# Optimization experiments

Hardware: AMD Instinct MI355X
Metric: run time of the kernel (lower is better)

The kernel has to match this reference:

```python
import jax, jax.numpy as jnp
import numpy as np

N = 50000       # num nodes
E = 800000      # num edges (avg degree 16)
D_IN = 128
D_H = 128
D_LAT = 64
BN_EPS = 1e-5


def _glorot(key, fan_in, fan_out):
    return jax.random.normal(key, (fan_in, fan_out), jnp.float32) / np.sqrt(fan_in).astype(np.float32)


def setup_inputs() -> dict:
    key = jax.random.key(0)
    ks = jax.random.split(key, 8)
    x = jax.random.normal(ks[0], (N, D_IN), jnp.float32)
    edge_index = jax.random.randint(ks[1], (2, E), 0, N)  # row 0 = src, row 1 = dst
    return {
        "x": x,
        "edge_index": edge_index,
        "W0": _glorot(ks[2], D_IN, D_H),
        "W1": _glorot(ks[3], D_H, D_H),
        "W_mu": _glorot(ks[4], D_H, D_LAT),
        "W_logvar": _glorot(ks[5], D_H, D_LAT),
        "gamma0": jnp.ones((D_H,), jnp.float32),
        "beta0": jnp.zeros((D_H,), jnp.float32),
        "gamma1": jnp.ones((D_H,), jnp.float32),
        "beta1": jnp.zeros((D_H,), jnp.float32),
    }


def _gcn_conv(h, W, src, dst, dinv):
    # Standard GCN with self-loops: D^{-1/2}(A+I)D^{-1/2} (X W)
    m = h @ W                                   # [N, out]
    coef = (dinv[src] * dinv[dst])[:, None]     # [E, 1]
    out = jax.ops.segment_sum(m[src] * coef, dst, num_segments=N)
    return out + m * (dinv * dinv)[:, None]     # self-loop contribution


def _batchnorm(h, gamma, beta):
    mean = jnp.mean(h, axis=0)
    var = jnp.var(h, axis=0)
    return (h - mean) * jax.lax.rsqrt(var + BN_EPS) * gamma + beta


def reference(x, edge_index, W0, W1, W_mu, W_logvar, gamma0, beta0, gamma1, beta1):
    # decoder_type='graph', augment_type=None, used_edge_weight=False,
    # use_FCencoder=False, num_domains=1; dropout is identity in reference.
    src, dst = edge_index[0], edge_index[1]
    deg = jax.ops.segment_sum(jnp.ones((E,), x.dtype), dst, num_segments=N) + 1.0
    dinv = jax.lax.rsqrt(deg)

    h = _gcn_conv(x, W0, src, dst, dinv)
    h = jax.nn.relu(_batchnorm(h, gamma0, beta0))
    h = _gcn_conv(h, W1, src, dst, dinv)
    h = jax.nn.relu(_batchnorm(h, gamma1, beta1))

    z_mean = _gcn_conv(h, W_mu, src, dst, dinv)
    z_log_std = _gcn_conv(h, W_logvar, src, dst, dinv)
    return (z_mean, z_log_std)
```

## Files before the change

### kernel.cpp

```cpp
#include <hip/hip_runtime.h>
#include <hip/hip_bf16.h>


using short8 = __attribute__((ext_vector_type(8))) short;
using f32x4  = __attribute__((ext_vector_type(4))) float;

static __device__ __forceinline__ unsigned short f2bf(float f) {
    __hip_bfloat16 h = __float2bfloat16(f);
    return *reinterpret_cast<unsigned short*>(&h);
}
static __device__ __forceinline__ float bf_lo(unsigned int u) {
    return __uint_as_float(u << 16);
}
static __device__ __forceinline__ float bf_hi(unsigned int u) {
    return __uint_as_float(u & 0xffff0000u);
}
static __device__ __forceinline__ float bf2f(unsigned short u) {
    return __uint_as_float((unsigned int)u << 16);
}

__global__ __launch_bounds__(256)
void deg_count(const int* __restrict__ ei, int* __restrict__ cnt, int E_) {
    int e = blockIdx.x * 256 + threadIdx.x;
    if (e < E_) atomicAdd(&cnt[ei[E_ + e]], 1);
}

__global__ __launch_bounds__(1024)
void scan_blocks(const int* __restrict__ cnt, float* __restrict__ dinv,
                 int* __restrict__ rowptr, int* __restrict__ partials, int n) {
    __shared__ int ls[1024];
    int tid = threadIdx.x;
    int i = blockIdx.x * 1024 + tid;
    int v = (i < n) ? cnt[i] : 0;
    if (i < n) dinv[i] = rsqrtf((float)v + 1.0f);
    ls[tid] = v;
    __syncthreads();
    #pragma unroll
    for (int off = 1; off < 1024; off <<= 1) {
        int t = (tid >= off) ? ls[tid - off] : 0;
        __syncthreads();
        ls[tid] += t;
        __syncthreads();
    }
    if (i < n) rowptr[i] = ls[tid] - v;
    if (tid == 1023) partials[blockIdx.x] = ls[1023];
}

__global__ __launch_bounds__(1024)
void scan_partials(int* __restrict__ partials, int* __restrict__ rowptr_n,
                   int nb) {
    __shared__ int ls[1024];
    int tid = threadIdx.x;
    int v = (tid < nb) ? partials[tid] : 0;
    ls[tid] = v;
    __syncthreads();
    #pragma unroll
    for (int off = 1; off < 1024; off <<= 1) {
        int t = (tid >= off) ? ls[tid - off] : 0;
        __syncthreads();
        ls[tid] += t;
        __syncthreads();
    }
    if (tid < nb) partials[tid] = ls[tid] - v;
    if (tid == 1023) *rowptr_n = ls[1023];
}

__global__ __launch_bounds__(256)
void scan_add(int* __restrict__ rowptr, int* __restrict__ gcursor,
              const int* __restrict__ partials, int n) {
    int i = blockIdx.x * 256 + threadIdx.x;
    if (i < n) {
        int v = rowptr[i] + partials[i >> 10];
        rowptr[i] = v;
        if ((i & 127) == 0) gcursor[i >> 7] = v;
    }
}

#define BCHUNK 4096
__global__ __launch_bounds__(256)
void bin_edges(const int* __restrict__ ei, const float* __restrict__ dinv,
               int* __restrict__ gcursor, uint2* __restrict__ binned, int E_) {
    __shared__ int hist[512];
    __shared__ int gbase[512];
    __shared__ int cur[512];
    const int tid = threadIdx.x;
    const int e0 = blockIdx.x * BCHUNK;

    #pragma unroll
    for (int q = 0; q < 2; ++q) hist[q * 256 + tid] = 0;
    __syncthreads();

    for (int i = tid; i < BCHUNK; i += 256) {
        int e = e0 + i;
        if (e < E_) atomicAdd(&hist[ei[E_ + e] >> 7], 1);
    }
    __syncthreads();

    #pragma unroll
    for (int q = 0; q < 2; ++q) {
        int b = q * 256 + tid;
        int c = hist[b];
        gbase[b] = c ? atomicAdd(&gcursor[b], c) : 0;
        cur[b] = 0;
    }
    __syncthreads();

    for (int i = tid; i < BCHUNK; i += 256) {
        int e = e0 + i;
        if (e >= E_) continue;
        int s = ei[e], d = ei[E_ + e];
        float coef = dinv[s] * dinv[d];
        unsigned int cb = (__float_as_uint(coef) + 0x8000u) >> 16;
        unsigned int entry = ((unsigned int)s << 15) | (cb & 0x7fffu);
        int b = d >> 7;
        int p = gbase[b] + atomicAdd(&cur[b], 1);
        binned[p] = make_uint2(entry, (unsigned int)(d & 127));
    }
}

__global__ __launch_bounds__(256)
void place_edges(const uint2* __restrict__ binned, const int* __restrict__ rowptr,
                 unsigned int* __restrict__ csr, int n) {
    __shared__ int cur[128];
    const int tid = threadIdx.x;
    const int n0 = blockIdx.x * 128;
    const int nn = min(128, n - n0);
    if (tid < nn) cur[tid] = rowptr[n0 + tid];
    __syncthreads();
    const int beg = rowptr[n0];
    const int end = rowptr[min(n0 + 128, n)];
    for (int i = beg + tid; i < end; i += 256) {
        uint2 v = binned[i];
        int p = atomicAdd(&cur[v.y], 1);
        csr[p] = v.x;
    }
}

template<bool XBF, bool FUSE_BN, bool SPLIT_W>
__global__ __launch_bounds__(256)
void gemm_mfma(const void* __restrict__ Xv, const float* __restrict__ Wa,
               const float* __restrict__ Wb, const float* __restrict__ sc,
               const float* __restrict__ sh, unsigned short* __restrict__ Y,
               int nRows) {
    __shared__ unsigned short wt[128 * 128];

    const int tid = threadIdx.x;

    #pragma unroll
    for (int it = 0; it < 16; ++it) {
        int flat4 = it * 256 + tid;
        int k  = flat4 >> 5;
        int c0 = (flat4 & 31) * 4;
        const float* srcp;
        if (!SPLIT_W) srcp = Wa + k * 128 + c0;
        else          srcp = (c0 < 64) ? (Wa + k * 64 + c0)
                                       : (Wb + k * 64 + (c0 - 64));
        float4 v = *(const float4*)srcp;
        float vv[4] = {v.x, v.y, v.z, v.w};
        #pragma unroll
        for (int j = 0; j < 4; ++j) {
            int c = c0 + j;
            wt[c * 128 + (k ^ ((c & 7) << 3))] = f2bf(vv[j]);
        }
    }
    __syncthreads();

    const int lane = tid & 63;
    const int wv   = tid >> 6;
    const int lm   = lane & 15;
    const int lg   = lane >> 4;
    const int row0 = blockIdx.x * 128 + wv * 32;

    f32x4 acc[2][8] = {};

    #pragma unroll
    for (int ks = 0; ks < 4; ++ks) {
        const int k0 = ks * 32 + lg * 8;

        short8 a[2];
        #pragma unroll
        for (int mf = 0; mf < 2; ++mf) {
            int r = row0 + mf * 16 + lm;
            if (r < nRows) {
                if (XBF) {
                    a[mf] = *(const short8*)((const unsigned short*)Xv +
                                             (size_t)r * 128 + k0);
                    if (FUSE_BN) {
                        float4 s0 = *(const float4*)(sc + k0);
                        float4 s1 = *(const float4*)(sc + k0 + 4);
                        float4 h0 = *(const float4*)(sh + k0);
                        float4 h1 = *(const float4*)(sh + k0 + 4);
                        float sv[8] = {s0.x, s0.y, s0.z, s0.w, s1.x, s1.y, s1.z, s1.w};
                        float hv[8] = {h0.x, h0.y, h0.z, h0.w, h1.x, h1.y, h1.z, h1.w};
                        #pragma unroll
                        for (int j = 0; j < 8; ++j) {
                            float v = bf2f((unsigned short)a[mf][j]);
                            v = fmaxf(v * sv[j] + hv[j], 0.f);
                            a[mf][j] = (short)f2bf(v);
                        }
                    }
                } else {
                    const float* xp = (const float*)Xv + (size_t)r * 128 + k0;
                    float4 p0 = *(const float4*)xp;
                    float4 p1 = *(const float4*)(xp + 4);
                    float pv[8] = {p0.x, p0.y, p0.z, p0.w, p1.x, p1.y, p1.z, p1.w};
                    #pragma unroll
                    for (int j = 0; j < 8; ++j) a[mf][j] = (short)f2bf(pv[j]);
                }
            } else {
                a[mf] = short8{};
            }
        }

        #pragma unroll
        for (int f = 0; f < 8; ++f) {
            int c = f * 16 + lm;
            short8 b = *(const short8*)&wt[c * 128 + (k0 ^ ((c & 7) << 3))];
            acc[0][f] = __builtin_amdgcn_mfma_f32_16x16x32_bf16(a[0], b, acc[0][f], 0, 0, 0);
            acc[1][f] = __builtin_amdgcn_mfma_f32_16x16x32_bf16(a[1], b, acc[1][f], 0, 0, 0);
        }
    }

    #pragma unroll
    for (int mf = 0; mf < 2; ++mf) {
        #pragma unroll
        for (int reg = 0; reg < 4; ++reg) {
            int r = row0 + mf * 16 + lg * 4 + reg;
            if (r >= nRows) continue;
            #pragma unroll
            for (int f = 0; f < 8; ++f)
                Y[(size_t)r * 128 + f * 16 + lm] = f2bf(acc[mf][f][reg]);
        }
    }
}

template<bool TO_OUT>
__global__ __launch_bounds__(256)
void gather_bf(const unsigned short* __restrict__ M,
               const int* __restrict__ rowptr,
               const unsigned int* __restrict__ csr,
               const float* __restrict__ dinv, void* __restrict__ O, int n) {
    int wid  = (blockIdx.x * 256 + threadIdx.x) >> 6;
    int lane = threadIdx.x & 63;
    if (wid >= n) return;
    const unsigned int* m2 = (const unsigned int*)M;

    float di = dinv[wid];
    unsigned int su = m2[(size_t)wid * 64 + lane];
    float c = di * di;
    float a0x = bf_lo(su) * c, a0y = bf_hi(su) * c;
    float a1x = 0.f, a1y = 0.f, a2x = 0.f, a2y = 0.f, a3x = 0.f, a3y = 0.f;

    int beg = __builtin_amdgcn_readfirstlane(rowptr[wid]);
    int end = __builtin_amdgcn_readfirstlane(rowptr[wid + 1]);

    int k = beg;
    for (; k + 3 < end; k += 4) {
        unsigned int e0 = csr[k],     e1 = csr[k + 1];
        unsigned int e2 = csr[k + 2], e3 = csr[k + 3];
        unsigned int u0 = m2[(size_t)(e0 >> 15) * 64 + lane];
        unsigned int u1 = m2[(size_t)(e1 >> 15) * 64 + lane];
        unsigned int u2 = m2[(size_t)(e2 >> 15) * 64 + lane];
        unsigned int u3 = m2[(size_t)(e3 >> 15) * 64 + lane];
        float w0 = __uint_as_float((e0 & 0x7fffu) << 16);
        float w1 = __uint_as_float((e1 & 0x7fffu) << 16);
        float w2 = __uint_as_float((e2 & 0x7fffu) << 16);
        float w3 = __uint_as_float((e3 & 0x7fffu) << 16);
        a0x += w0 * bf_lo(u0); a0y += w0 * bf_hi(u0);
        a1x += w1 * bf_lo(u1); a1y += w1 * bf_hi(u1);
        a2x += w2 * bf_lo(u2); a2y += w2 * bf_hi(u2);
        a3x += w3 * bf_lo(u3); a3y += w3 * bf_hi(u3);
    }
    for (; k < end; ++k) {
        unsigned int e0 = csr[k];
        unsigned int u0 = m2[(size_t)(e0 >> 15) * 64 + lane];
        float w0 = __uint_as_float((e0 & 0x7fffu) << 16);
        a0x += w0 * bf_lo(u0); a0y += w0 * bf_hi(u0);
    }
    float ax = (a0x + a1x) + (a2x + a3x);
    float ay = (a0y + a1y) + (a2y + a3y);

    if (!TO_OUT) {
        unsigned int o = (unsigned int)f2bf(ax) | ((unsigned int)f2bf(ay) << 16);
        ((unsigned int*)O)[(size_t)wid * 64 + lane] = o;
    } else {
        float* Of = (float*)O;
        float* dst = (lane < 32)
            ? Of + (size_t)wid * 64 + 2 * lane
            : Of + (size_t)n * 64 + (size_t)wid * 64 + 2 * (lane - 32);
        *(float2*)dst = make_float2(ax, ay);
    }
}

__global__ __launch_bounds__(256)
void bn_stats(const unsigned short* __restrict__ H, float* __restrict__ stats,
              const float* __restrict__ gamma, const float* __restrict__ beta,
              float* __restrict__ sc, float* __restrict__ sh,
              unsigned int* __restrict__ ticket, int n) {
    const uint4* h4 = (const uint4*)H;
    const int tid = threadIdx.x;
    const int cg = tid & 15;
    const int rg = tid >> 4;
    float s[8] = {}, q[8] = {};
    for (int r = blockIdx.x * 16 + rg; r < n; r += gridDim.x * 16) {
        uint4 u = h4[(size_t)r * 16 + cg];
        float v[8] = {bf_lo(u.x), bf_hi(u.x), bf_lo(u.y), bf_hi(u.y),
                      bf_lo(u.z), bf_hi(u.z), bf_lo(u.w), bf_hi(u.w)};
        #pragma unroll
        for (int j = 0; j < 8; ++j) { s[j] += v[j]; q[j] += v[j] * v[j]; }
    }
    __shared__ float ls[256][17];
    #pragma unroll
    for (int j = 0; j < 8; ++j) { ls[tid][j] = s[j]; ls[tid][8 + j] = q[j]; }
    __syncthreads();
    if (tid < 128) {
        int cgrp = tid >> 3, j = tid & 7;
        float S = 0.f, Q = 0.f;
        #pragma unroll
        for (int g = 0; g < 16; ++g) {
            S += ls[(g << 4) | cgrp][j];
            Q += ls[(g << 4) | cgrp][8 + j];
        }
        atomicAdd(&stats[tid], S);
        atomicAdd(&stats[128 + tid], Q);
    }
    __syncthreads();
    __shared__ int lastFlag;
    if (tid == 0) {
        __threadfence();
        unsigned int t = atomicAdd(ticket, 1u);
        lastFlag = (t == gridDim.x - 1);
    }
    __syncthreads();
    if (lastFlag && tid < 128) {
        float Ssum = __hip_atomic_load(&stats[tid], __ATOMIC_RELAXED,
                                       __HIP_MEMORY_SCOPE_AGENT);
        float Qsum = __hip_atomic_load(&stats[128 + tid], __ATOMIC_RELAXED,
                                       __HIP_MEMORY_SCOPE_AGENT);
        float inv_n = 1.0f / (float)n;
        float mean = Ssum * inv_n;
        float var  = Qsum * inv_n - mean * mean;
        float sv = rsqrtf(var + 1e-5f) * gamma[tid];
        sc[tid] = sv;
        sh[tid] = beta[tid] - mean * sv;
    }
}

extern "C" void kernel_launch(void* const* d_in, const int* in_sizes, int n_in,
                              void* d_out, int out_size, void* d_ws, size_t ws_size,
                              hipStream_t stream) {
    const float* x    = (const float*)d_in[0];
    const int*   ei   = (const int*)d_in[1];
    const float* W0   = (const float*)d_in[2];
    const float* W1   = (const float*)d_in[3];
    const float* Wmu  = (const float*)d_in[4];
    const float* Wlog = (const float*)d_in[5];
    const float* g0   = (const float*)d_in[6];
    const float* b0   = (const float*)d_in[7];
    const float* g1   = (const float*)d_in[8];
    const float* b1   = (const float*)d_in[9];

    const int N_ = in_sizes[0] / 128;
    const int E_ = in_sizes[1] / 2;
    float* out = (float*)d_out;

    char* w = (char*)d_ws;
    auto carve = [&](size_t bytes) {
        char* p = w;
        w += (bytes + 255) & ~(size_t)255;
        return p;
    };
    int*   cnt     = (int*)  carve((size_t)N_ * 4);
    float* stats0  = (float*)carve(256 * 4);
    float* stats1  = (float*)carve(256 * 4);
    unsigned int* ticket0 = (unsigned int*)carve(256);
    unsigned int* ticket1 = (unsigned int*)carve(256);
    char*  zend    = w;
    float* dinv    = (float*)carve((size_t)N_ * 4);
    int*   rowptr  = (int*)  carve((size_t)(N_ + 1) * 4);
    int*   gcursor = (int*)  carve(512 * 4);
    int*   partials= (int*)  carve(1024 * 4);
    unsigned int* csr = (unsigned int*)carve((size_t)E_ * 4);
    uint2* binned  = (uint2*)carve((size_t)E_ * 8);
    float* sc0     = (float*)carve(128 * 4);
    float* sh0     = (float*)carve(128 * 4);
    float* sc1     = (float*)carve(128 * 4);
    float* sh1     = (float*)carve(128 * 4);
    unsigned short* Mbf = (unsigned short*)carve((size_t)N_ * 128 * 2);
    unsigned short* Hb  = (unsigned short*)carve((size_t)N_ * 128 * 2);

    const int gGemm = (N_ + 127) / 128;
    const int gGath = (N_ * 64 + 255) / 256;
    const int nb    = (N_ + 1023) / 1024;
    const int nbk   = (N_ + 127) / 128;
    const int gBin  = (E_ + BCHUNK - 1) / BCHUNK;

    hipMemsetAsync(cnt, 0, (size_t)(zend - (char*)cnt), stream);
    deg_count<<<(E_ + 255) / 256, 256, 0, stream>>>(ei, cnt, E_);
    scan_blocks<<<nb, 1024, 0, stream>>>(cnt, dinv, rowptr, partials, N_);
    scan_partials<<<1, 1024, 0, stream>>>(partials, rowptr + N_, nb);
    scan_add<<<(N_ + 255) / 256, 256, 0, stream>>>(rowptr, gcursor, partials, N_);
    bin_edges<<<gBin, 256, 0, stream>>>(ei, dinv, gcursor, binned, E_);
    place_edges<<<nbk, 256, 0, stream>>>(binned, rowptr, csr, N_);

    gemm_mfma<false, false, false><<<gGemm, 256, 0, stream>>>(
        x, W0, nullptr, nullptr, nullptr, Mbf, N_);
    gather_bf<false><<<gGath, 256, 0, stream>>>(Mbf, rowptr, csr, dinv, Hb, N_);
    bn_stats<<<512, 256, 0, stream>>>(Hb, stats0, g0, b0, sc0, sh0, ticket0, N_);

    gemm_mfma<true, true, false><<<gGemm, 256, 0, stream>>>(
        Hb, W1, nullptr, sc0, sh0, Mbf, N_);
    gather_bf<false><<<gGath, 256, 0, stream>>>(Mbf, rowptr, csr, dinv, Hb, N_);
    bn_stats<<<512, 256, 0, stream>>>(Hb, stats1, g1, b1, sc1, sh1, ticket1, N_);

    gemm_mfma<true, true, true><<<gGemm, 256, 0, stream>>>(
        Hb, Wmu, Wlog, sc1, sh1, Mbf, N_);
    gather_bf<true><<<gGath, 256, 0, stream>>>(Mbf, rowptr, csr, dinv, out, N_);
}
```

Measured before the change: 259.1 us.

## Split feature matrices into four column slabs for cache-local gathers

```diff
diff --git a/kernel.cpp b/kernel.cpp
--- a/kernel.cpp
+++ b/kernel.cpp
@@ -183,8 +183,9 @@
             int r = row0 + mf * 16 + lm;
             if (r < nRows) {
                 if (XBF) {
-                    a[mf] = *(const short8*)((const unsigned short*)Xv +
-                                             (size_t)r * 128 + k0);
+                    const unsigned short* X = (const unsigned short*)Xv;
+                    a[mf] = *(const short8*)(X +
+                        ((size_t)(k0 >> 5) * nRows + r) * 32 + (k0 & 31));
                     if (FUSE_BN) {
                         float4 s0 = *(const float4*)(sc + k0);
                         float4 s1 = *(const float4*)(sc + k0 + 4);
@@ -228,66 +229,62 @@
             int r = row0 + mf * 16 + lg * 4 + reg;
             if (r >= nRows) continue;
             #pragma unroll
-            for (int f = 0; f < 8; ++f)
-                Y[(size_t)r * 128 + f * 16 + lm] = f2bf(acc[mf][f][reg]);
+            for (int f = 0; f < 8; ++f) {
+                int c = f * 16 + lm;
+                Y[((size_t)(c >> 5) * nRows + r) * 32 + (c & 31)] =
+                    f2bf(acc[mf][f][reg]);
+            }
         }
     }
 }
 
 template<bool TO_OUT>
 __global__ __launch_bounds__(256)
-void gather_bf(const unsigned short* __restrict__ M,
-               const int* __restrict__ rowptr,
-               const unsigned int* __restrict__ csr,
-               const float* __restrict__ dinv, void* __restrict__ O, int n) {
-    int wid  = (blockIdx.x * 256 + threadIdx.x) >> 6;
-    int lane = threadIdx.x & 63;
-    if (wid >= n) return;
-    const unsigned int* m2 = (const unsigned int*)M;
-
-    float di = dinv[wid];
-    unsigned int su = m2[(size_t)wid * 64 + lane];
+void gather_q(const unsigned short* __restrict__ M,
+              const int* __restrict__ rowptr,
+              const unsigned int* __restrict__ csr,
+              const float* __restrict__ dinv, void* __restrict__ O, int n) {
+    const int tid  = threadIdx.x;
+    const int q    = blockIdx.x & 3;
+    const int tile = blockIdx.x >> 2;
+    const int l16  = tid & 15;
+    const int node = tile * 16 + (tid >> 4);
+    if (node >= n) return;
+
+    const unsigned int* slab = (const unsigned int*)M + (size_t)q * n * 16;
+
+    float di = dinv[node];
+    unsigned int su = slab[(size_t)node * 16 + l16];
     float c = di * di;
     float a0x = bf_lo(su) * c, a0y = bf_hi(su) * c;
-    float a1x = 0.f, a1y = 0.f, a2x = 0.f, a2y = 0.f, a3x = 0.f, a3y = 0.f;
-
-    int beg = __builtin_amdgcn_readfirstlane(rowptr[wid]);
-    int end = __builtin_amdgcn_readfirstlane(rowptr[wid + 1]);
-
+    float a1x = 0.f, a1y = 0.f;
+
+    int beg = rowptr[node], end = rowptr[node + 1];
     int k = beg;
-    for (; k + 3 < end; k += 4) {
-        unsigned int e0 = csr[k],     e1 = csr[k + 1];
-        unsigned int e2 = csr[k + 2], e3 = csr[k + 3];
-        unsigned int u0 = m2[(size_t)(e0 >> 15) * 64 + lane];
-        unsigned int u1 = m2[(size_t)(e1 >> 15) * 64 + lane];
-        unsigned int u2 = m2[(size_t)(e2 >> 15) * 64 + lane];
-        unsigned int u3 = m2[(size_t)(e3 >> 15) * 64 + lane];
+    for (; k + 1 < end; k += 2) {
+        unsigned int e0 = csr[k], e1 = csr[k + 1];
+        unsigned int u0 = slab[(size_t)(e0 >> 15) * 16 + l16];
+        unsigned int u1 = slab[(size_t)(e1 >> 15) * 16 + l16];
         float w0 = __uint_as_float((e0 & 0x7fffu) << 16);
         float w1 = __uint_as_float((e1 & 0x7fffu) << 16);
-        float w2 = __uint_as_float((e2 & 0x7fffu) << 16);
-        float w3 = __uint_as_float((e3 & 0x7fffu) << 16);
         a0x += w0 * bf_lo(u0); a0y += w0 * bf_hi(u0);
         a1x += w1 * bf_lo(u1); a1y += w1 * bf_hi(u1);
-        a2x += w2 * bf_lo(u2); a2y += w2 * bf_hi(u2);
-        a3x += w3 * bf_lo(u3); a3y += w3 * bf_hi(u3);
-    }
-    for (; k < end; ++k) {
+    }
+    if (k < end) {
         unsigned int e0 = csr[k];
-        unsigned int u0 = m2[(size_t)(e0 >> 15) * 64 + lane];
+        unsigned int u0 = slab[(size_t)(e0 >> 15) * 16 + l16];
         float w0 = __uint_as_float((e0 & 0x7fffu) << 16);
         a0x += w0 * bf_lo(u0); a0y += w0 * bf_hi(u0);
     }
-    float ax = (a0x + a1x) + (a2x + a3x);
-    float ay = (a0y + a1y) + (a2y + a3y);
+    float ax = a0x + a1x;
+    float ay = a0y + a1y;
 
     if (!TO_OUT) {
         unsigned int o = (unsigned int)f2bf(ax) | ((unsigned int)f2bf(ay) << 16);
-        ((unsigned int*)O)[(size_t)wid * 64 + lane] = o;
+        ((unsigned int*)O)[(size_t)q * n * 16 + (size_t)node * 16 + l16] = o;
     } else {
-        float* Of = (float*)O;
-        float* dst = (lane < 32)
-            ? Of + (size_t)wid * 64 + 2 * lane
-            : Of + (size_t)n * 64 + (size_t)wid * 64 + 2 * (lane - 32);
+        float* dst = (float*)O + (size_t)(q >> 1) * n * 64 +
+                     (size_t)node * 64 + (q & 1) * 32 + 2 * l16;
         *(float2*)dst = make_float2(ax, ay);
     }
 }
@@ -297,32 +294,35 @@
               const float* __restrict__ gamma, const float* __restrict__ beta,
               float* __restrict__ sc, float* __restrict__ sh,
               unsigned int* __restrict__ ticket, int n) {
-    const uint4* h4 = (const uint4*)H;
     const int tid = threadIdx.x;
-    const int cg = tid & 15;
-    const int rg = tid >> 4;
-    float s[8] = {}, q[8] = {};
-    for (int r = blockIdx.x * 16 + rg; r < n; r += gridDim.x * 16) {
-        uint4 u = h4[(size_t)r * 16 + cg];
+    const int q   = blockIdx.x & 3;
+    const int bq  = blockIdx.x >> 2;
+    const int nbq = gridDim.x >> 2;
+    const uint4* hq = (const uint4*)(H + (size_t)q * n * 32);
+    const int total = n * 4;
+    float s[8] = {}, qq[8] = {};
+    for (int f = bq * 256 + tid; f < total; f += nbq * 256) {
+        uint4 u = hq[f];
         float v[8] = {bf_lo(u.x), bf_hi(u.x), bf_lo(u.y), bf_hi(u.y),
                       bf_lo(u.z), bf_hi(u.z), bf_lo(u.w), bf_hi(u.w)};
         #pragma unroll
-        for (int j = 0; j < 8; ++j) { s[j] += v[j]; q[j] += v[j] * v[j]; }
+        for (int j = 0; j < 8; ++j) { s[j] += v[j]; qq[j] += v[j] * v[j]; }
     }
     __shared__ float ls[256][17];
     #pragma unroll
-    for (int j = 0; j < 8; ++j) { ls[tid][j] = s[j]; ls[tid][8 + j] = q[j]; }
-    __syncthreads();
-    if (tid < 128) {
-        int cgrp = tid >> 3, j = tid & 7;
+    for (int j = 0; j < 8; ++j) { ls[tid][j] = s[j]; ls[tid][8 + j] = qq[j]; }
+    __syncthreads();
+    if (tid < 32) {
+        int wg = tid >> 3, j = tid & 7;
         float S = 0.f, Q = 0.f;
         #pragma unroll
-        for (int g = 0; g < 16; ++g) {
-            S += ls[(g << 4) | cgrp][j];
-            Q += ls[(g << 4) | cgrp][8 + j];
+        for (int g = 0; g < 64; ++g) {
+            S += ls[g * 4 + wg][j];
+            Q += ls[g * 4 + wg][8 + j];
         }
-        atomicAdd(&stats[tid], S);
-        atomicAdd(&stats[128 + tid], Q);
+        int ch = q * 32 + wg * 8 + j;
+        atomicAdd(&stats[ch], S);
+        atomicAdd(&stats[128 + ch], Q);
     }
     __syncthreads();
     __shared__ int lastFlag;
@@ -390,7 +390,7 @@
     unsigned short* Hb  = (unsigned short*)carve((size_t)N_ * 128 * 2);
 
     const int gGemm = (N_ + 127) / 128;
-    const int gGath = (N_ * 64 + 255) / 256;
+    const int gGath = ((N_ + 15) / 16) * 4;
     const int nb    = (N_ + 1023) / 1024;
     const int nbk   = (N_ + 127) / 128;
     const int gBin  = (E_ + BCHUNK - 1) / BCHUNK;
@@ -405,15 +405,15 @@
 
     gemm_mfma<false, false, false><<<gGemm, 256, 0, stream>>>(
         x, W0, nullptr, nullptr, nullptr, Mbf, N_);
-    gather_bf<false><<<gGath, 256, 0, stream>>>(Mbf, rowptr, csr, dinv, Hb, N_);
+    gather_q<false><<<gGath, 256, 0, stream>>>(Mbf, rowptr, csr, dinv, Hb, N_);
     bn_stats<<<512, 256, 0, stream>>>(Hb, stats0, g0, b0, sc0, sh0, ticket0, N_);
 
     gemm_mfma<true, true, false><<<gGemm, 256, 0, stream>>>(
         Hb, W1, nullptr, sc0, sh0, Mbf, N_);
-    gather_bf<false><<<gGath, 256, 0, stream>>>(Mbf, rowptr, csr, dinv, Hb, N_);
+    gather_q<false><<<gGath, 256, 0, stream>>>(Mbf, rowptr, csr, dinv, Hb, N_);
     bn_stats<<<512, 256, 0, stream>>>(Hb, stats1, g1, b1, sc1, sh1, ticket1, N_);
 
     gemm_mfma<true, true, true><<<gGemm, 256, 0, stream>>>(
         Hb, Wmu, Wlog, sc1, sh1, Mbf, N_);
-    gather_bf<true><<<gGath, 256, 0, stream>>>(Mbf, rowptr, csr, dinv, out, N_);
-}
+    gather_q<true><<<gGath, 256, 0, stream>>>(Mbf, rowptr, csr, dinv, out, N_);
+}
```

Result: slower. 304.9 us (+17.7%).
